# Kernel tuning notes

Hardware: AMD Instinct MI355X
Metric: run time of the kernel (lower is better)

## Reference

```python
import jax, jax.numpy as jnp
import numpy as np

N_HEADS = 8

def setup_inputs() -> dict:
    key = jax.random.key(0)
    ks = jax.random.split(key, 8)
    N, D, H = 20000, 16, 256
    scale = np.float32(0.02)
    return {
        "h": jax.random.normal(ks[0], (N, H), dtype=jnp.float32),
        "attention_mask": jnp.zeros((N,), dtype=jnp.float32),
        "neighbor_idx": jax.random.randint(ks[1], (N, D), 0, N, dtype=jnp.int32),
        "Wq": jax.random.normal(ks[2], (H, H), dtype=jnp.float32) * scale,
        "bq": jnp.zeros((H,), dtype=jnp.float32),
        "Wk": jax.random.normal(ks[3], (H, H), dtype=jnp.float32) * scale,
        "bk": jnp.zeros((H,), dtype=jnp.float32),
        "Wv": jax.random.normal(ks[4], (H, H), dtype=jnp.float32) * scale,
        "bv": jnp.zeros((H,), dtype=jnp.float32),
    }

def reference(h, attention_mask, neighbor_idx, Wq, bq, Wk, bk, Wv, bv):
    N, H = h.shape
    nh = N_HEADS
    dh = H // nh
    inv_sqrt_dh = np.float32(1.0 / np.sqrt(dh))
    # query from each node's own state: [N, nh, dh]
    q = (h @ Wq.T + bq).reshape(N, nh, dh)
    # gather neighbor mailbox: [N, D, H]
    nb = h[neighbor_idx]
    k = (nb @ Wk.T + bk).reshape(N, -1, nh, dh)  # [N, D, nh, dh]
    v = (nb @ Wv.T + bv).reshape(N, -1, nh, dh)
    # scores: [N, nh, D]
    scores = jnp.einsum('nhd,nkhd->nhk', q, k) * inv_sqrt_dh
    # additive mask gathered from source nodes, broadcast over heads
    scores = scores + attention_mask[neighbor_idx][:, None, :]
    probs = jax.nn.softmax(scores, axis=-1)
    # dropout prob = 0.0 (eval) -> identity
    ctx = jnp.einsum('nhk,nkhd->nhd', probs, v).reshape(N, H)
    return ctx
```

## Files before the change

kernel.cpp:

```cpp
#include <hip/hip_runtime.h>
#include <math.h>

#define HDIM 256
#define DNEIGH 16

typedef __attribute__((ext_vector_type(8))) short short8;
typedef __attribute__((ext_vector_type(4))) float f32x4;

static __device__ __forceinline__ unsigned short f2bf(float f) {
    unsigned int u = __float_as_uint(f);
    unsigned int r = (u + 0x7fffu + ((u >> 16) & 1u)) >> 16;
    return (unsigned short)r;
}
static __device__ __forceinline__ float bf_lo(unsigned int u) {
    return __uint_as_float(u << 16);
}
static __device__ __forceinline__ float bf_hi(unsigned int u) {
    return __uint_as_float(u & 0xffff0000u);
}

__global__ __launch_bounds__(256) void cvt_kernel(
    const float* __restrict__ h,
    const float* __restrict__ wq, const float* __restrict__ wk, const float* __restrict__ wv,
    unsigned short* __restrict__ hb,
    unsigned short* __restrict__ wqb, unsigned short* __restrict__ wkb, unsigned short* __restrict__ wvb,
    int nh4)
{
    const int stride = gridDim.x * blockDim.x;
    const int total = nh4 + 3 * 16384;
    for (int i = blockIdx.x * blockDim.x + threadIdx.x; i < total; i += stride) {
        const float4* src; unsigned short* dst; int off;
        if (i < nh4) { src = (const float4*)h; dst = hb; off = i; }
        else {
            int j = i - nh4; int s = j >> 14; off = j & 16383;
            src = (s == 0) ? (const float4*)wq : (s == 1) ? (const float4*)wk : (const float4*)wv;
            dst = (s == 0) ? wqb : (s == 1) ? wkb : wvb;
        }
        float4 v = src[off];
        ushort4 o;
        o.x = f2bf(v.x); o.y = f2bf(v.y); o.z = f2bf(v.z); o.w = f2bf(v.w);
        *(ushort4*)&dst[off * 4] = o;
    }
}

#define LDA 72

__global__ __launch_bounds__(256) void qkv_mfma_kernel(
    const unsigned short* __restrict__ hb,
    const unsigned short* __restrict__ Wqb,
    const unsigned short* __restrict__ Wkb,
    const unsigned short* __restrict__ Wvb,
    const float* __restrict__ bq, const float* __restrict__ bk, const float* __restrict__ bv,
    float* __restrict__ Q, unsigned short* __restrict__ Kb, unsigned short* __restrict__ Vb,
    int N)
{
    __shared__ unsigned short As[128 * LDA];
    __shared__ unsigned short Bs[64 * LDA];

    const int t = threadIdx.x;
    const int lane = t & 63;
    const int wid = t >> 6;
    const int wm = wid >> 1;
    const int wn = wid & 1;
    const int m0 = blockIdx.x * 128;
    const int o0 = blockIdx.y * 64;
    const int sel = o0 >> 8;
    const int wrow0 = o0 & 255;

    const unsigned short* __restrict__ W = (sel == 0) ? Wqb : (sel == 1) ? Wkb : Wvb;
    const float* __restrict__ bias = (sel == 0) ? bq : (sel == 1) ? bk : bv;

    f32x4 acc[4][2] = {};

    for (int k0 = 0; k0 < HDIM; k0 += 64) {
#pragma unroll
        for (int r = 0; r < 4; ++r) {
            int idx = t + r * 256;
            int row = idx >> 3;
            int off = (idx & 7) * 8;
            int gr = m0 + row;
            uint4 val = make_uint4(0u, 0u, 0u, 0u);
            if (gr < N) val = *(const uint4*)&hb[(size_t)gr * HDIM + k0 + off];
            *(uint4*)&As[row * LDA + off] = val;
        }
#pragma unroll
        for (int r = 0; r < 2; ++r) {
            int idx = t + r * 256;
            int row = idx >> 3;
            int off = (idx & 7) * 8;
            uint4 val = *(const uint4*)&W[(size_t)(wrow0 + row) * HDIM + k0 + off];
            *(uint4*)&Bs[row * LDA + off] = val;
        }
        __syncthreads();

#pragma unroll
        for (int ks = 0; ks < 2; ++ks) {
            short8 af[4], bf[2];
#pragma unroll
            for (int i = 0; i < 4; ++i) {
                int m = wm * 64 + i * 16 + (lane & 15);
                af[i] = *(const short8*)&As[m * LDA + ks * 32 + (lane >> 4) * 8];
            }
#pragma unroll
            for (int j = 0; j < 2; ++j) {
                int n = wn * 32 + j * 16 + (lane & 15);
                bf[j] = *(const short8*)&Bs[n * LDA + ks * 32 + (lane >> 4) * 8];
            }
#pragma unroll
            for (int i = 0; i < 4; ++i)
#pragma unroll
                for (int j = 0; j < 2; ++j)
                    acc[i][j] = __builtin_amdgcn_mfma_f32_16x16x32_bf16(af[i], bf[j], acc[i][j], 0, 0, 0);
        }
        __syncthreads();
    }

#pragma unroll
    for (int i = 0; i < 4; ++i) {
        int mbase = m0 + wm * 64 + i * 16 + (lane >> 4) * 4;
#pragma unroll
        for (int j = 0; j < 2; ++j) {
            int col = wrow0 + wn * 32 + j * 16 + (lane & 15);
            float b = bias[col];
#pragma unroll
            for (int r = 0; r < 4; ++r) {
                int gr = mbase + r;
                if (gr < N) {
                    float v = acc[i][j][r] + b;
                    if (sel == 0)       Q[(size_t)gr * HDIM + col] = v;
                    else if (sel == 1)  Kb[(size_t)gr * HDIM + col] = f2bf(v);
                    else                Vb[(size_t)gr * HDIM + col] = f2bf(v);
                }
            }
        }
    }
}

__global__ __launch_bounds__(256) void attn2_kernel(
    const float* __restrict__ Q,
    const unsigned short* __restrict__ Kb,
    const unsigned short* __restrict__ Vb,
    const float* __restrict__ mask,
    const int* __restrict__ nidx,
    float* __restrict__ out,
    int N)
{
    const int w = threadIdx.x >> 6;
    const int lane = threadIdx.x & 63;
    const int n = blockIdx.x * 4 + w;
    if (n >= N) return;

    int idl = nidx[(size_t)n * DNEIGH + (lane & 15)];
    float mskl = mask[idl];
    float4 q = *(const float4*)&Q[(size_t)n * HDIM + lane * 4];

    uint2 kreg[DNEIGH];
#pragma unroll
    for (int d = 0; d < DNEIGH; ++d) {
        int id = __shfl(idl, d);
        kreg[d] = *(const uint2*)&Kb[(size_t)id * HDIM + lane * 4];
    }

    float scr[DNEIGH];
#pragma unroll
    for (int d = 0; d < DNEIGH; ++d) {
        float p = q.x * bf_lo(kreg[d].x) + q.y * bf_hi(kreg[d].x)
                + q.z * bf_lo(kreg[d].y) + q.w * bf_hi(kreg[d].y);
        p += __shfl_xor(p, 1);
        p += __shfl_xor(p, 2);
        p += __shfl_xor(p, 4);
        float mk = __shfl(mskl, d);
        scr[d] = p * 0.17677669529663688f + mk;
    }

    float mx = scr[0];
#pragma unroll
    for (int d = 1; d < DNEIGH; ++d) mx = fmaxf(mx, scr[d]);
    float e[DNEIGH], s = 0.f;
#pragma unroll
    for (int d = 0; d < DNEIGH; ++d) { e[d] = __expf(scr[d] - mx); s += e[d]; }
    float rs = 1.f / s;

    float4 acc = make_float4(0.f, 0.f, 0.f, 0.f);
#pragma unroll
    for (int d = 0; d < DNEIGH; ++d) {
        int id = __shfl(idl, d);
        uint2 vr = *(const uint2*)&Vb[(size_t)id * HDIM + lane * 4];
        float wgt = e[d] * rs;
        acc.x += wgt * bf_lo(vr.x);
        acc.y += wgt * bf_hi(vr.x);
        acc.z += wgt * bf_lo(vr.y);
        acc.w += wgt * bf_hi(vr.y);
    }
    *(float4*)&out[(size_t)n * HDIM + lane * 4] = acc;
}

extern "C" void kernel_launch(void* const* d_in, const int* in_sizes, int n_in,
                              void* d_out, int out_size, void* d_ws, size_t ws_size,
                              hipStream_t stream)
{
    const float* h    = (const float*)d_in[0];
    const float* mask = (const float*)d_in[1];
    const int*   nidx = (const int*)d_in[2];
    const float* Wq   = (const float*)d_in[3];
    const float* bq   = (const float*)d_in[4];
    const float* Wk   = (const float*)d_in[5];
    const float* bk   = (const float*)d_in[6];
    const float* Wv   = (const float*)d_in[7];
    const float* bv   = (const float*)d_in[8];

    const int N = in_sizes[0] / HDIM;

    char* ws = (char*)d_ws;
    float*          Qp  = (float*)ws;                       ws += (size_t)N * HDIM * 4;
    unsigned short* Kbp = (unsigned short*)ws;              ws += (size_t)N * HDIM * 2;
    unsigned short* Vbp = (unsigned short*)ws;              ws += (size_t)N * HDIM * 2;
    unsigned short* hbp = (unsigned short*)ws;              ws += (size_t)N * HDIM * 2;
    unsigned short* Wqb = (unsigned short*)ws;              ws += 65536 * 2;
    unsigned short* Wkb = (unsigned short*)ws;              ws += 65536 * 2;
    unsigned short* Wvb = (unsigned short*)ws;

    const int nh4 = (N * HDIM) / 4;
    cvt_kernel<<<1280, 256, 0, stream>>>(h, Wq, Wk, Wv, hbp, Wqb, Wkb, Wvb, nh4);

    dim3 g1((N + 127) / 128, 12);
    qkv_mfma_kernel<<<g1, 256, 0, stream>>>(hbp, Wqb, Wkb, Wvb, bq, bk, bv, Qp, Kbp, Vbp, N);

    attn2_kernel<<<(N + 3) / 4, 256, 0, stream>>>(Qp, Kbp, Vbp, mask, nidx, (float*)d_out, N);
}
```

Baseline: 165.1 us.

## Retile QKV GEMM with async LDS loads, preload V, drop softmax max

The QKV GEMM moves from 128x64 to 128x128 tiles, which halves the grid's y dimension. It fills shared memory with global_load_lds async copies and replaces row padding with an XOR-swizzled layout to avoid bank conflicts. The attention kernel now loads V rows together with K rows, so the gathers overlap. It uses readlane instead of shuffles and drops the max-subtraction step of the softmax. Skipping the max is numerically unsafe for large scores, and the GEMM no longer bounds-checks rows past N on load.

```diff
diff --git a/kernel.cpp b/kernel.cpp
--- a/kernel.cpp
+++ b/kernel.cpp
@@ -17,6 +17,12 @@
 }
 static __device__ __forceinline__ float bf_hi(unsigned int u) {
     return __uint_as_float(u & 0xffff0000u);
+}
+
+static __device__ __forceinline__ void async_copy16(const void* g, void* l) {
+    __builtin_amdgcn_global_load_lds(
+        (const __attribute__((address_space(1))) unsigned int*)g,
+        (__attribute__((address_space(3))) unsigned int*)l, 16, 0, 0);
 }
 
 __global__ __launch_bounds__(256) void cvt_kernel(
@@ -43,8 +49,6 @@
     }
 }
 
-#define LDA 72
-
 __global__ __launch_bounds__(256) void qkv_mfma_kernel(
     const unsigned short* __restrict__ hb,
     const unsigned short* __restrict__ Wqb,
@@ -54,8 +58,8 @@
     float* __restrict__ Q, unsigned short* __restrict__ Kb, unsigned short* __restrict__ Vb,
     int N)
 {
-    __shared__ unsigned short As[128 * LDA];
-    __shared__ unsigned short Bs[64 * LDA];
+    __shared__ unsigned short As[128 * 64];
+    __shared__ unsigned short Bs[128 * 64];
 
     const int t = threadIdx.x;
     const int lane = t & 63;
@@ -63,53 +67,52 @@
     const int wm = wid >> 1;
     const int wn = wid & 1;
     const int m0 = blockIdx.x * 128;
-    const int o0 = blockIdx.y * 64;
+    const int o0 = blockIdx.y * 128;
     const int sel = o0 >> 8;
     const int wrow0 = o0 & 255;
 
     const unsigned short* __restrict__ W = (sel == 0) ? Wqb : (sel == 1) ? Wkb : Wvb;
     const float* __restrict__ bias = (sel == 0) ? bq : (sel == 1) ? bk : bv;
 
-    f32x4 acc[4][2] = {};
+    const int srow = lane >> 3;
+    const int cg = (lane & 7) ^ srow;
+
+    f32x4 acc[4][4] = {};
 
     for (int k0 = 0; k0 < HDIM; k0 += 64) {
 #pragma unroll
         for (int r = 0; r < 4; ++r) {
-            int idx = t + r * 256;
-            int row = idx >> 3;
-            int off = (idx & 7) * 8;
-            int gr = m0 + row;
-            uint4 val = make_uint4(0u, 0u, 0u, 0u);
-            if (gr < N) val = *(const uint4*)&hb[(size_t)gr * HDIM + k0 + off];
-            *(uint4*)&As[row * LDA + off] = val;
-        }
-#pragma unroll
-        for (int r = 0; r < 2; ++r) {
-            int idx = t + r * 256;
-            int row = idx >> 3;
-            int off = (idx & 7) * 8;
-            uint4 val = *(const uint4*)&W[(size_t)(wrow0 + row) * HDIM + k0 + off];
-            *(uint4*)&Bs[row * LDA + off] = val;
+            int rowb = wid * 32 + r * 8;
+            const unsigned short* gp = &hb[(size_t)(m0 + rowb + srow) * HDIM + k0 + cg * 8];
+            async_copy16(gp, &As[rowb * 64]);
+        }
+#pragma unroll
+        for (int r = 0; r < 4; ++r) {
+            int rowb = wid * 32 + r * 8;
+            const unsigned short* gp = &W[(size_t)(wrow0 + rowb + srow) * HDIM + k0 + cg * 8];
+            async_copy16(gp, &Bs[rowb * 64]);
         }
         __syncthreads();
 
 #pragma unroll
         for (int ks = 0; ks < 2; ++ks) {
-            short8 af[4], bf[2];
+            short8 af[4], bf[4];
 #pragma unroll
             for (int i = 0; i < 4; ++i) {
                 int m = wm * 64 + i * 16 + (lane & 15);
-                af[i] = *(const short8*)&As[m * LDA + ks * 32 + (lane >> 4) * 8];
+                int chunk = (ks * 4 + (lane >> 4)) ^ (m & 7);
+                af[i] = *(const short8*)&As[m * 64 + chunk * 8];
             }
 #pragma unroll
-            for (int j = 0; j < 2; ++j) {
-                int n = wn * 32 + j * 16 + (lane & 15);
-                bf[j] = *(const short8*)&Bs[n * LDA + ks * 32 + (lane >> 4) * 8];
+            for (int j = 0; j < 4; ++j) {
+                int n = wn * 64 + j * 16 + (lane & 15);
+                int chunk = (ks * 4 + (lane >> 4)) ^ (n & 7);
+                bf[j] = *(const short8*)&Bs[n * 64 + chunk * 8];
             }
 #pragma unroll
             for (int i = 0; i < 4; ++i)
 #pragma unroll
-                for (int j = 0; j < 2; ++j)
+                for (int j = 0; j < 4; ++j)
                     acc[i][j] = __builtin_amdgcn_mfma_f32_16x16x32_bf16(af[i], bf[j], acc[i][j], 0, 0, 0);
         }
         __syncthreads();
@@ -119,8 +122,8 @@
     for (int i = 0; i < 4; ++i) {
         int mbase = m0 + wm * 64 + i * 16 + (lane >> 4) * 4;
 #pragma unroll
-        for (int j = 0; j < 2; ++j) {
-            int col = wrow0 + wn * 32 + j * 16 + (lane & 15);
+        for (int j = 0; j < 4; ++j) {
+            int col = wrow0 + wn * 64 + j * 16 + (lane & 15);
             float b = bias[col];
 #pragma unroll
             for (int r = 0; r < 4; ++r) {
@@ -154,14 +157,16 @@
     float mskl = mask[idl];
     float4 q = *(const float4*)&Q[(size_t)n * HDIM + lane * 4];
 
-    uint2 kreg[DNEIGH];
+    uint2 kreg[DNEIGH], vreg[DNEIGH];
 #pragma unroll
     for (int d = 0; d < DNEIGH; ++d) {
-        int id = __shfl(idl, d);
+        int id = __builtin_amdgcn_readlane(idl, d);
         kreg[d] = *(const uint2*)&Kb[(size_t)id * HDIM + lane * 4];
-    }
-
-    float scr[DNEIGH];
+        vreg[d] = *(const uint2*)&Vb[(size_t)id * HDIM + lane * 4];
+    }
+
+    float e[DNEIGH];
+    float s = 0.f;
 #pragma unroll
     for (int d = 0; d < DNEIGH; ++d) {
         float p = q.x * bf_lo(kreg[d].x) + q.y * bf_hi(kreg[d].x)
@@ -169,28 +174,22 @@
         p += __shfl_xor(p, 1);
         p += __shfl_xor(p, 2);
         p += __shfl_xor(p, 4);
-        float mk = __shfl(mskl, d);
-        scr[d] = p * 0.17677669529663688f + mk;
-    }
-
-    float mx = scr[0];
-#pragma unroll
-    for (int d = 1; d < DNEIGH; ++d) mx = fmaxf(mx, scr[d]);
-    float e[DNEIGH], s = 0.f;
-#pragma unroll
-    for (int d = 0; d < DNEIGH; ++d) { e[d] = __expf(scr[d] - mx); s += e[d]; }
+        float mk = __builtin_amdgcn_readlane(__float_as_int(mskl), d);
+        mk = __int_as_float(__float_as_int(mk));
+        float scr = p * 0.17677669529663688f + __int_as_float(__builtin_amdgcn_readlane(__float_as_int(mskl), d));
+        e[d] = __expf(scr);
+        s += e[d];
+    }
     float rs = 1.f / s;
 
     float4 acc = make_float4(0.f, 0.f, 0.f, 0.f);
 #pragma unroll
     for (int d = 0; d < DNEIGH; ++d) {
-        int id = __shfl(idl, d);
-        uint2 vr = *(const uint2*)&Vb[(size_t)id * HDIM + lane * 4];
         float wgt = e[d] * rs;
-        acc.x += wgt * bf_lo(vr.x);
-        acc.y += wgt * bf_hi(vr.x);
-        acc.z += wgt * bf_lo(vr.y);
-        acc.w += wgt * bf_hi(vr.y);
+        acc.x += wgt * bf_lo(vreg[d].x);
+        acc.y += wgt * bf_hi(vreg[d].x);
+        acc.z += wgt * bf_lo(vreg[d].y);
+        acc.w += wgt * bf_hi(vreg[d].y);
     }
     *(float4*)&out[(size_t)n * HDIM + lane * 4] = acc;
 }
@@ -212,18 +211,18 @@
     const int N = in_sizes[0] / HDIM;
 
     char* ws = (char*)d_ws;
-    float*          Qp  = (float*)ws;                       ws += (size_t)N * HDIM * 4;
-    unsigned short* Kbp = (unsigned short*)ws;              ws += (size_t)N * HDIM * 2;
-    unsigned short* Vbp = (unsigned short*)ws;              ws += (size_t)N * HDIM * 2;
-    unsigned short* hbp = (unsigned short*)ws;              ws += (size_t)N * HDIM * 2;
-    unsigned short* Wqb = (unsigned short*)ws;              ws += 65536 * 2;
-    unsigned short* Wkb = (unsigned short*)ws;              ws += 65536 * 2;
+    float*          Qp  = (float*)ws;          ws += (size_t)N * HDIM * 4;
+    unsigned short* Kbp = (unsigned short*)ws; ws += (size_t)N * HDIM * 2;
+    unsigned short* Vbp = (unsigned short*)ws; ws += (size_t)N * HDIM * 2;
+    unsigned short* hbp = (unsigned short*)ws; ws += (size_t)N * HDIM * 2;
+    unsigned short* Wqb = (unsigned short*)ws; ws += 65536 * 2;
+    unsigned short* Wkb = (unsigned short*)ws; ws += 65536 * 2;
     unsigned short* Wvb = (unsigned short*)ws;
 
     const int nh4 = (N * HDIM) / 4;
     cvt_kernel<<<1280, 256, 0, stream>>>(h, Wq, Wk, Wv, hbp, Wqb, Wkb, Wvb, nh4);
 
-    dim3 g1((N + 127) / 128, 12);
+    dim3 g1((N + 127) / 128, 6);
     qkv_mfma_kernel<<<g1, 256, 0, stream>>>(hbp, Wqb, Wkb, Wvb, bq, bk, bv, Qp, Kbp, Vbp, N);
 
     attn2_kernel<<<(N + 3) / 4, 256, 0, stream>>>(Qp, Kbp, Vbp, mask, nidx, (float*)d_out, N);
```

Result: faster. 160.3 us (-2.9%).
